# Performance work log

Measured on AMD Instinct MI355X. Metric: run time of the kernel, lower is better.

The kernel has to match this reference:

```python
import jax, jax.numpy as jnp
import numpy as np

B, D, U, M, K = 8192, 512, 512, 16, 64


def setup_inputs() -> dict:
    key = jax.random.key(0)
    ks = jax.random.split(key, 5)
    return {
        "x": jax.random.normal(ks[0], (B, D), dtype=jnp.float32),
        "key_kernel": jax.random.normal(ks[1], (D, K), dtype=jnp.float32) * (1.0 / np.sqrt(D)),
        "key_bias": jnp.zeros((K,), dtype=jnp.float32),
        "keys_map": jax.random.normal(ks[2], (M, K), dtype=jnp.float32),
        "kernels": jax.random.normal(ks[3], (M, D, U), dtype=jnp.float32) * (1.0 / np.sqrt(D)),
        "biases": jnp.zeros((M, U), dtype=jnp.float32),
    }


def reference(x, key_kernel, key_bias, keys_map, kernels, biases):
    # key projection: [B, K]
    keyv = x @ key_kernel + key_bias
    # inverse-distance similarity to mode keys: [B, M]
    dist = jnp.sqrt(jnp.sum((keyv[:, None, :] - keys_map[None, :, :]) ** 2, axis=-1))
    sim = 1.0 / (dist + 1.0)
    modes = kernels.shape[0]
    # kernel = mean_m(sim_m * kernels_m); out = x @ kernel.
    # Distributive identity: out = (1/M) * sum_m sim_m * (x @ kernels_m)
    out = jnp.einsum("bm,bd,mdu->bu", sim, x, kernels) / modes
    # bias = mean_m(sim_m * biases_m): [B, U]
    out = out + (sim @ biases) / modes
    return out
```

## Files before the change

### kernel.cpp

```cpp
#include <hip/hip_runtime.h>
#include <hip/hip_bf16.h>
#include <stdint.h>

#define B_SZ 8192
#define D_SZ 512
#define U_SZ 512
#define M_SZ 16
#define K_SZ 64

typedef short bf16x8 __attribute__((ext_vector_type(8)));
typedef float f32x4 __attribute__((ext_vector_type(4)));

__device__ __forceinline__ unsigned short f2bf(float f) {
  union { float f; unsigned u; } v; v.f = f;
  unsigned r = v.u + 0x7fffu + ((v.u >> 16) & 1u);
  return (unsigned short)(r >> 16);
}

__global__ __launch_bounds__(256) void prep1(
    const float* __restrict__ x, const float* __restrict__ key_kernel,
    const float* __restrict__ kernels, unsigned short* __restrict__ xbf,
    unsigned short* __restrict__ kbf, unsigned short* __restrict__ wkbf) {
  __shared__ float tf[32][65];
  int bid = blockIdx.x;
  int t = threadIdx.x;

  if (bid < 2048) {
    int m = bid >> 7;
    int rem = bid & 127;
    int a = (rem >> 3) & 15;
    int ut = rem & 7;
    int d0 = a * 32, u0 = ut * 64;
    {
      int dr = t >> 4, uc = t & 15;
      const float* src = kernels + ((size_t)m * D_SZ + d0 + dr) * U_SZ + u0 + uc * 4;
      float4 aa = *(const float4*)src;
      float4 bb = *(const float4*)(src + (size_t)16 * U_SZ);
      tf[dr][uc * 4 + 0] = aa.x; tf[dr][uc * 4 + 1] = aa.y;
      tf[dr][uc * 4 + 2] = aa.z; tf[dr][uc * 4 + 3] = aa.w;
      tf[dr + 16][uc * 4 + 0] = bb.x; tf[dr + 16][uc * 4 + 1] = bb.y;
      tf[dr + 16][uc * 4 + 2] = bb.z; tf[dr + 16][uc * 4 + 3] = bb.w;
    }
    __syncthreads();
    {
      int ur = t >> 2, dc = t & 3;
      int j = ur >> 4, lane16 = ur & 15;
      int kt = a >> 1, h = a & 1;
      unsigned short* dst = kbf +
          (((((size_t)m * 8 + ut) * 8 + kt) * 4 + j) * 2 + h) * 512 +
          ((size_t)dc * 16 + lane16) * 8;
      ushort4 lo, hi;
      lo.x = f2bf(tf[dc * 8 + 0][ur]); lo.y = f2bf(tf[dc * 8 + 1][ur]);
      lo.z = f2bf(tf[dc * 8 + 2][ur]); lo.w = f2bf(tf[dc * 8 + 3][ur]);
      hi.x = f2bf(tf[dc * 8 + 4][ur]); hi.y = f2bf(tf[dc * 8 + 5][ur]);
      hi.z = f2bf(tf[dc * 8 + 6][ur]); hi.w = f2bf(tf[dc * 8 + 7][ur]);
      *(ushort4*)dst = lo;
      *(ushort4*)(dst + 4) = hi;
    }
    return;
  }

  if (bid < 2056) {
    int kt = bid - 2048;
#pragma unroll
    for (int rep = 0; rep < 2; ++rep) {
      int c = rep * 256 + t;
      int j = c >> 7, h = (c >> 6) & 1, quad = (c >> 4) & 3, ln = c & 15;
      int dd = kt * 64 + h * 32 + quad * 8;
      int u = j * 16 + ln;
      unsigned short v[8];
#pragma unroll
      for (int e = 0; e < 8; ++e)
        v[e] = f2bf(key_kernel[(size_t)(dd + e) * K_SZ + u]);
      unsigned short* dst =
          wkbf + ((size_t)((kt * 4 + j) * 2 + h) * 64 + quad * 16 + ln) * 8;
#pragma unroll
      for (int e = 0; e < 8; ++e) dst[e] = v[e];
    }
    return;
  }

  int xb0 = bid - 2056;
  int bt = xb0 >> 3, i = xb0 & 7;
  int b0 = xb0 * 16;
#pragma unroll
  for (int rep = 0; rep < 4; ++rep) {
    int idx = rep * 256 + t;
    int kt = idx >> 7, h = (idx >> 6) & 1, quad = (idx >> 4) & 3, ln = idx & 15;
    const float* src = x + (size_t)(b0 + ln) * D_SZ + kt * 64 + h * 32 + quad * 8;
    float4 a = *(const float4*)src;
    float4 b = *(const float4*)(src + 4);
    ushort4 lo, hi;
    lo.x = f2bf(a.x); lo.y = f2bf(a.y); lo.z = f2bf(a.z); lo.w = f2bf(a.w);
    hi.x = f2bf(b.x); hi.y = f2bf(b.y); hi.z = f2bf(b.z); hi.w = f2bf(b.w);
    unsigned short* dst =
        xbf + ((((size_t)bt * 8 + kt) * 8 + i) * 2 + h) * 512 +
        ((size_t)quad * 16 + ln) * 8;
    *(ushort4*)dst = lo;
    *(ushort4*)(dst + 4) = hi;
  }
}

__global__ __launch_bounds__(256) void prep2(
    const unsigned short* __restrict__ xbf, const unsigned short* __restrict__ wkbf,
    const float* __restrict__ key_bias, const float* __restrict__ keys_map,
    float* __restrict__ simT) {
  __shared__ float kv[64][68];
  __shared__ float sKM[16][64];
  int t = threadIdx.x, w = t >> 6, l = t & 63;
  int blk = blockIdx.x;
  int b0 = blk * 64, bt = blk >> 1, ibase = (blk & 1) * 4;
  int lane16 = l & 15, quad = l >> 4;

  ((float4*)sKM)[t] = ((const float4*)keys_map)[t];

  f32x4 acc[4];
#pragma unroll
  for (int j = 0; j < 4; ++j) acc[j] = (f32x4){0.f, 0.f, 0.f, 0.f};

  for (int kt = 0; kt < 8; ++kt) {
    bf16x8 af[2];
#pragma unroll
    for (int h = 0; h < 2; ++h)
      af[h] = *(const bf16x8*)(xbf +
                               ((((size_t)bt * 8 + kt) * 8 + ibase + w) * 2 + h) * 512 +
                               (size_t)l * 8);
#pragma unroll
    for (int j = 0; j < 4; ++j) {
      bf16x8 b0f = *(const bf16x8*)(wkbf + ((size_t)((kt * 4 + j) * 2 + 0) * 64 + l) * 8);
      bf16x8 b1f = *(const bf16x8*)(wkbf + ((size_t)((kt * 4 + j) * 2 + 1) * 64 + l) * 8);
      acc[j] = __builtin_amdgcn_mfma_f32_16x16x32_bf16(af[0], b0f, acc[j], 0, 0, 0);
      acc[j] = __builtin_amdgcn_mfma_f32_16x16x32_bf16(af[1], b1f, acc[j], 0, 0, 0);
    }
  }
#pragma unroll
  for (int j = 0; j < 4; ++j) {
    float bc = key_bias[j * 16 + lane16];
#pragma unroll
    for (int r = 0; r < 4; ++r)
      kv[w * 16 + quad * 4 + r][j * 16 + lane16] = acc[j][r] + bc;
  }
  __syncthreads();

  int row = t >> 2, mg = (t & 3) * 4;
  float d2[4] = {0.f, 0.f, 0.f, 0.f};
#pragma unroll 8
  for (int k = 0; k < 64; ++k) {
    float kvv = kv[row][k];
#pragma unroll
    for (int q = 0; q < 4; ++q) {
      float df = kvv - sKM[mg + q][k];
      d2[q] += df * df;
    }
  }
#pragma unroll
  for (int q = 0; q < 4; ++q)
    simT[(size_t)(mg + q) * B_SZ + b0 + row] = 1.0f / (sqrtf(d2[q]) + 1.0f);
}

__global__ __launch_bounds__(256, 2) void poly_gemm(
    const unsigned short* __restrict__ xbf,
    const unsigned short* __restrict__ kbf,
    const float* __restrict__ simT,
    const float* __restrict__ biases,
    float* __restrict__ out) {
  __shared__ float sRed[8192];

  int t = threadIdx.x, w = t >> 6, l = t & 63;
  int bid = blockIdx.x;
  int ut = bid & 7, bt = bid >> 3;
  int b0 = bt * 128, u0 = ut * 64;
  int half = w >> 1, rw = w & 1;
  int lane16 = l & 15, quad = l >> 4;

  f32x4 facc[4][4];
#pragma unroll
  for (int i = 0; i < 4; ++i)
#pragma unroll
    for (int j = 0; j < 4; ++j) facc[i][j] = (f32x4){0.f, 0.f, 0.f, 0.f};

#pragma unroll 1
  for (int kt = 0; kt < 8; ++kt) {
    bf16x8 af[4][2];
#pragma unroll
    for (int ii = 0; ii < 4; ++ii)
#pragma unroll
      for (int h = 0; h < 2; ++h)
        af[ii][h] = *(const bf16x8*)(
            xbf + ((((size_t)bt * 8 + kt) * 8 + rw * 4 + ii) * 2 + h) * 512 +
            (size_t)l * 8);

#pragma unroll 2
    for (int mi = 0; mi < 8; ++mi) {
      int mode = half * 8 + mi;
      const unsigned short* bb =
          kbf + ((((size_t)mode * 8 + ut) * 8 + kt) * 4) * 2 * 512;
      bf16x8 bfr[4][2];
#pragma unroll
      for (int j = 0; j < 4; ++j)
#pragma unroll
        for (int h = 0; h < 2; ++h)
          bfr[j][h] = *(const bf16x8*)(bb + ((size_t)(j * 2 + h)) * 512 +
                                       (size_t)l * 8);

      f32x4 sv[4];
#pragma unroll
      for (int i = 0; i < 4; ++i)
        sv[i] = *(const f32x4*)(simT + (size_t)mode * B_SZ + b0 + rw * 64 +
                                i * 16 + quad * 4);

#pragma unroll
      for (int i = 0; i < 4; ++i)
#pragma unroll
        for (int j = 0; j < 4; ++j) {
          f32x4 p = __builtin_amdgcn_mfma_f32_16x16x32_bf16(
              af[i][0], bfr[j][0], (f32x4){0.f, 0.f, 0.f, 0.f}, 0, 0, 0);
          p = __builtin_amdgcn_mfma_f32_16x16x32_bf16(af[i][1], bfr[j][1], p,
                                                      0, 0, 0);
#pragma unroll
          for (int r = 0; r < 4; ++r) facc[i][j][r] += sv[i][r] * p[r];
        }

      if (kt == 0) {
        float bbv[4];
#pragma unroll
        for (int j = 0; j < 4; ++j)
          bbv[j] = biases[(size_t)mode * U_SZ + u0 + j * 16 + lane16];
#pragma unroll
        for (int i = 0; i < 4; ++i)
#pragma unroll
          for (int j = 0; j < 4; ++j)
#pragma unroll
            for (int r = 0; r < 4; ++r) facc[i][j][r] += sv[i][r] * bbv[j];
      }
    }
  }

  __syncthreads();
  if (half == 1) {
#pragma unroll
    for (int i = 0; i < 4; ++i)
#pragma unroll
      for (int r = 0; r < 4; ++r)
#pragma unroll
        for (int j = 0; j < 4; ++j)
          sRed[rw * 4096 + (i * 16 + quad * 4 + r) * 64 + j * 16 + lane16] =
              facc[i][j][r];
  }
  __syncthreads();
  if (half == 0) {
#pragma unroll
    for (int i = 0; i < 4; ++i)
#pragma unroll
      for (int r = 0; r < 4; ++r) {
        int row = b0 + rw * 64 + i * 16 + quad * 4 + r;
        float* orow = out + (size_t)row * U_SZ + u0;
#pragma unroll
        for (int j = 0; j < 4; ++j)
          orow[j * 16 + lane16] =
              (facc[i][j][r] +
               sRed[rw * 4096 + (i * 16 + quad * 4 + r) * 64 + j * 16 + lane16]) *
              0.0625f;
      }
  }
}

extern "C" void kernel_launch(void* const* d_in, const int* in_sizes, int n_in,
                              void* d_out, int out_size, void* d_ws, size_t ws_size,
                              hipStream_t stream) {
  const float* x = (const float*)d_in[0];
  const float* key_kernel = (const float*)d_in[1];
  const float* key_bias = (const float*)d_in[2];
  const float* keys_map = (const float*)d_in[3];
  const float* kernels = (const float*)d_in[4];
  const float* biases = (const float*)d_in[5];
  float* out = (float*)d_out;

  char* p = (char*)d_ws;
  unsigned short* xbf = (unsigned short*)p;  p += (size_t)B_SZ * D_SZ * 2;
  unsigned short* kbf = (unsigned short*)p;  p += (size_t)M_SZ * U_SZ * D_SZ * 2;
  unsigned short* wkbf = (unsigned short*)p; p += (size_t)K_SZ * D_SZ * 2;
  float* simT = (float*)p;

  prep1<<<dim3(2568), 256, 0, stream>>>(x, key_kernel, kernels, xbf, kbf, wkbf);
  prep2<<<dim3(128), 256, 0, stream>>>(xbf, wkbf, key_bias, keys_map, simT);
  poly_gemm<<<dim3(512), 256, 0, stream>>>(xbf, kbf, simT, biases, out);
}
```

Measured before the change: 172.2 us.

## Split poly_gemm modes across four wave pairs with 512-thread blocks

Doubles the block size of the main GEMM kernel from 256 to 512 threads so that four wave pairs each handle four of the sixteen modes instead of two pairs handling eight. This raises the number of waves per tile and shortens each wave's serial mode loop. The partial accumulators are then combined through a padded shared-memory buffer in a three-step serialized reduction. The extra barriers and reduction passes add cost, and register pressure under launch_bounds(512,4) may cause spills.

Result: slower. 520.2 us (+202.2%).

```diff
diff --git a/kernel.cpp b/kernel.cpp
--- a/kernel.cpp
+++ b/kernel.cpp
@@ -158,19 +158,19 @@
     simT[(size_t)(mg + q) * B_SZ + b0 + row] = 1.0f / (sqrtf(d2[q]) + 1.0f);
 }
 
-__global__ __launch_bounds__(256, 2) void poly_gemm(
+__global__ __launch_bounds__(512, 4) void poly_gemm(
     const unsigned short* __restrict__ xbf,
     const unsigned short* __restrict__ kbf,
     const float* __restrict__ simT,
     const float* __restrict__ biases,
     float* __restrict__ out) {
-  __shared__ float sRed[8192];
+  __shared__ float sRed[2][64][68];
 
   int t = threadIdx.x, w = t >> 6, l = t & 63;
   int bid = blockIdx.x;
   int ut = bid & 7, bt = bid >> 3;
   int b0 = bt * 128, u0 = ut * 64;
-  int half = w >> 1, rw = w & 1;
+  int q = w >> 1, rw = w & 1;
   int lane16 = l & 15, quad = l >> 4;
 
   f32x4 facc[4][4];
@@ -191,8 +191,8 @@
             (size_t)l * 8);
 
 #pragma unroll 2
-    for (int mi = 0; mi < 8; ++mi) {
-      int mode = half * 8 + mi;
+    for (int mi = 0; mi < 4; ++mi) {
+      int mode = q * 4 + mi;
       const unsigned short* bb =
           kbf + ((((size_t)mode * 8 + ut) * 8 + kt) * 4) * 2 * 512;
       bf16x8 bfr[4][2];
@@ -237,18 +237,37 @@
   }
 
   __syncthreads();
-  if (half == 1) {
+  if (q == 3) {
 #pragma unroll
     for (int i = 0; i < 4; ++i)
 #pragma unroll
       for (int r = 0; r < 4; ++r)
 #pragma unroll
         for (int j = 0; j < 4; ++j)
-          sRed[rw * 4096 + (i * 16 + quad * 4 + r) * 64 + j * 16 + lane16] =
-              facc[i][j][r];
-  }
-  __syncthreads();
-  if (half == 0) {
+          sRed[rw][i * 16 + quad * 4 + r][j * 16 + lane16] = facc[i][j][r];
+  }
+  __syncthreads();
+  if (q == 2) {
+#pragma unroll
+    for (int i = 0; i < 4; ++i)
+#pragma unroll
+      for (int r = 0; r < 4; ++r)
+#pragma unroll
+        for (int j = 0; j < 4; ++j)
+          sRed[rw][i * 16 + quad * 4 + r][j * 16 + lane16] += facc[i][j][r];
+  }
+  __syncthreads();
+  if (q == 1) {
+#pragma unroll
+    for (int i = 0; i < 4; ++i)
+#pragma unroll
+      for (int r = 0; r < 4; ++r)
+#pragma unroll
+        for (int j = 0; j < 4; ++j)
+          sRed[rw][i * 16 + quad * 4 + r][j * 16 + lane16] += facc[i][j][r];
+  }
+  __syncthreads();
+  if (q == 0) {
 #pragma unroll
     for (int i = 0; i < 4; ++i)
 #pragma unroll
@@ -259,7 +278,7 @@
         for (int j = 0; j < 4; ++j)
           orow[j * 16 + lane16] =
               (facc[i][j][r] +
-               sRed[rw * 4096 + (i * 16 + quad * 4 + r) * 64 + j * 16 + lane16]) *
+               sRed[rw][i * 16 + quad * 4 + r][j * 16 + lane16]) *
               0.0625f;
       }
   }
@@ -284,5 +303,5 @@
 
   prep1<<<dim3(2568), 256, 0, stream>>>(x, key_kernel, kernels, xbf, kbf, wkbf);
   prep2<<<dim3(128), 256, 0, stream>>>(xbf, wkbf, key_bias, keys_map, simT);
-  poly_gemm<<<dim3(512), 256, 0, stream>>>(xbf, kbf, simT, biases, out);
-}
+  poly_gemm<<<dim3(512), 512, 0, stream>>>(xbf, kbf, simT, biases, out);
+}
```

## Double-buffer weight tiles into LDS via async global_load_lds

Applied to the files above, without the earlier changes.

The GEMM kernel now streams each per-wave weight slice into a private double-buffered LDS region using global_load_lds, prefetching the next mode/k-tile while computing the current one, with manual vmcnt waits. Similarity and bias values are staged once into shared memory instead of being reloaded from global memory inside the inner loop. The reduction buffer gets padded rows to avoid bank conflicts. LDS use grows to about 76KB and the occupancy hint of 2 is dropped, which may reduce waves per CU. The hand-coded vmcnt counts also depend on the compiler not reordering the other vector-memory loads.

New measurement: 172.7 us. No clear change (+0.3%).

```diff
diff --git a/kernel.cpp b/kernel.cpp
--- a/kernel.cpp
+++ b/kernel.cpp
@@ -158,13 +158,23 @@
     simT[(size_t)(mg + q) * B_SZ + b0 + row] = 1.0f / (sqrtf(d2[q]) + 1.0f);
 }
 
-__global__ __launch_bounds__(256, 2) void poly_gemm(
+__device__ __forceinline__ void stage_slice(const unsigned short* src,
+                                            unsigned short* dst_lds) {
+#pragma unroll
+  for (int c = 0; c < 8; ++c)
+    __builtin_amdgcn_global_load_lds(
+        (const __attribute__((address_space(1))) unsigned int*)(src + c * 512),
+        (__attribute__((address_space(3))) unsigned int*)(dst_lds + c * 512),
+        16, 0, 0);
+}
+
+__global__ __launch_bounds__(256) void poly_gemm(
     const unsigned short* __restrict__ xbf,
     const unsigned short* __restrict__ kbf,
     const float* __restrict__ simT,
     const float* __restrict__ biases,
     float* __restrict__ out) {
-  __shared__ float sRed[8192];
+  __shared__ __align__(16) char smem[77824];
 
   int t = threadIdx.x, w = t >> 6, l = t & 63;
   int bid = blockIdx.x;
@@ -173,11 +183,32 @@
   int half = w >> 1, rw = w & 1;
   int lane16 = l & 15, quad = l >> 4;
 
+  float* sSim = (float*)(smem + 65536);
+  float* sBias = (float*)(smem + 73728);
+  unsigned short* kbuf = (unsigned short*)(smem + w * 16384);
+
+  {
+    int m = t >> 4, c = (t & 15) * 8;
+    const float* src = simT + (size_t)m * B_SZ + b0 + c;
+    float4 a = *(const float4*)src;
+    float4 b = *(const float4*)(src + 4);
+    float4* dst = (float4*)(sSim + m * 128 + c);
+    dst[0] = a; dst[1] = b;
+    int cb = (t & 15) * 4;
+    *(float4*)(sBias + m * 64 + cb) =
+        *(const float4*)(biases + (size_t)m * U_SZ + u0 + cb);
+  }
+  __syncthreads();
+
   f32x4 facc[4][4];
 #pragma unroll
   for (int i = 0; i < 4; ++i)
 #pragma unroll
     for (int j = 0; j < 4; ++j) facc[i][j] = (f32x4){0.f, 0.f, 0.f, 0.f};
+
+  const unsigned short* kbf_l = kbf + (size_t)l * 8;
+
+  stage_slice(kbf_l + ((((size_t)(half * 8) * 8 + ut) * 8) + 0) * 4096, kbuf);
 
 #pragma unroll 1
   for (int kt = 0; kt < 8; ++kt) {
@@ -190,24 +221,33 @@
             xbf + ((((size_t)bt * 8 + kt) * 8 + rw * 4 + ii) * 2 + h) * 512 +
             (size_t)l * 8);
 
-#pragma unroll 2
+#pragma unroll
     for (int mi = 0; mi < 8; ++mi) {
       int mode = half * 8 + mi;
-      const unsigned short* bb =
-          kbf + ((((size_t)mode * 8 + ut) * 8 + kt) * 4) * 2 * 512;
+      {
+        int nmi = (mi + 1) & 7;
+        int nkt = (mi == 7) ? ((kt + 1) & 7) : kt;
+        stage_slice(
+            kbf_l + ((((size_t)(half * 8 + nmi) * 8 + ut) * 8) + nkt) * 4096,
+            kbuf + ((mi + 1) & 1) * 4096);
+      }
+      if (mi == 0)
+        asm volatile("s_waitcnt vmcnt(16)" ::: "memory");
+      else
+        asm volatile("s_waitcnt vmcnt(8)" ::: "memory");
+
+      const unsigned short* lb = kbuf + (mi & 1) * 4096;
       bf16x8 bfr[4][2];
 #pragma unroll
       for (int j = 0; j < 4; ++j)
 #pragma unroll
         for (int h = 0; h < 2; ++h)
-          bfr[j][h] = *(const bf16x8*)(bb + ((size_t)(j * 2 + h)) * 512 +
-                                       (size_t)l * 8);
+          bfr[j][h] = *(const bf16x8*)(lb + (j * 2 + h) * 512 + (size_t)l * 8);
 
       f32x4 sv[4];
 #pragma unroll
       for (int i = 0; i < 4; ++i)
-        sv[i] = *(const f32x4*)(simT + (size_t)mode * B_SZ + b0 + rw * 64 +
-                                i * 16 + quad * 4);
+        sv[i] = *(const f32x4*)(sSim + mode * 128 + rw * 64 + i * 16 + quad * 4);
 
 #pragma unroll
       for (int i = 0; i < 4; ++i)
@@ -225,7 +265,7 @@
         float bbv[4];
 #pragma unroll
         for (int j = 0; j < 4; ++j)
-          bbv[j] = biases[(size_t)mode * U_SZ + u0 + j * 16 + lane16];
+          bbv[j] = sBias[mode * 64 + j * 16 + lane16];
 #pragma unroll
         for (int i = 0; i < 4; ++i)
 #pragma unroll
@@ -236,7 +276,10 @@
     }
   }
 
+  asm volatile("s_waitcnt vmcnt(0)" ::: "memory");
   __syncthreads();
+
+  float* sRed = (float*)smem;
   if (half == 1) {
 #pragma unroll
     for (int i = 0; i < 4; ++i)
@@ -244,7 +287,7 @@
       for (int r = 0; r < 4; ++r)
 #pragma unroll
         for (int j = 0; j < 4; ++j)
-          sRed[rw * 4096 + (i * 16 + quad * 4 + r) * 64 + j * 16 + lane16] =
+          sRed[(rw * 64 + i * 16 + quad * 4 + r) * 68 + j * 16 + lane16] =
               facc[i][j][r];
   }
   __syncthreads();
@@ -259,7 +302,7 @@
         for (int j = 0; j < 4; ++j)
           orow[j * 16 + lane16] =
               (facc[i][j][r] +
-               sRed[rw * 4096 + (i * 16 + quad * 4 + r) * 64 + j * 16 + lane16]) *
+               sRed[(rw * 64 + i * 16 + quad * 4 + r) * 68 + j * 16 + lane16]) *
               0.0625f;
       }
   }
```

## Stage mode kernels in LDS via async global_load_lds with a 4-buffer ring, larger batch tile

Applied to the files above, without the earlier changes.

Each poly_gemm block now covers 256 batch rows, with each wave owning 64 rows across all 16 modes. This removes the cross-half reduction through shared memory and halves the grid. Kernel tiles are streamed into a 4-deep LDS ring with global_load_lds, and the next x fragments are prefetched into registers, so loads overlap the MFMA work. Similarity and bias values are preloaded into LDS. Separately, the x bf16 conversion in prep1 now goes through an LDS transpose for coalesced reads. The costs are occupancy (1 block per CU with about 52 KB of LDS, grid of only 256 blocks) and fragile hand-written vmcnt waits.

Measured after the change: 183.3 us. 6.5% more time.

```diff
diff --git a/kernel.cpp b/kernel.cpp
--- a/kernel.cpp
+++ b/kernel.cpp
@@ -22,6 +22,7 @@
     const float* __restrict__ kernels, unsigned short* __restrict__ xbf,
     unsigned short* __restrict__ kbf, unsigned short* __restrict__ wkbf) {
   __shared__ float tf[32][65];
+  __shared__ unsigned short sx[16][520];
   int bid = blockIdx.x;
   int t = threadIdx.x;
 
@@ -80,24 +81,35 @@
     return;
   }
 
-  int xb0 = bid - 2056;
-  int bt = xb0 >> 3, i = xb0 & 7;
-  int b0 = xb0 * 16;
-#pragma unroll
-  for (int rep = 0; rep < 4; ++rep) {
-    int idx = rep * 256 + t;
-    int kt = idx >> 7, h = (idx >> 6) & 1, quad = (idx >> 4) & 3, ln = idx & 15;
-    const float* src = x + (size_t)(b0 + ln) * D_SZ + kt * 64 + h * 32 + quad * 8;
-    float4 a = *(const float4*)src;
-    float4 b = *(const float4*)(src + 4);
-    ushort4 lo, hi;
-    lo.x = f2bf(a.x); lo.y = f2bf(a.y); lo.z = f2bf(a.z); lo.w = f2bf(a.w);
-    hi.x = f2bf(b.x); hi.y = f2bf(b.y); hi.z = f2bf(b.z); hi.w = f2bf(b.w);
-    unsigned short* dst =
-        xbf + ((((size_t)bt * 8 + kt) * 8 + i) * 2 + h) * 512 +
-        ((size_t)quad * 16 + ln) * 8;
-    *(ushort4*)dst = lo;
-    *(ushort4*)(dst + 4) = hi;
+  {
+    int xb0 = bid - 2056;
+    int btx = xb0 >> 3, i = xb0 & 7;
+    int b0 = xb0 * 16;
+#pragma unroll
+    for (int rep = 0; rep < 8; ++rep) {
+      int idx = rep * 256 + t;
+      int row = idx >> 7;
+      int c4 = (idx & 127) * 4;
+      float4 v = *(const float4*)(x + (size_t)(b0 + row) * D_SZ + c4);
+      ushort4 o;
+      o.x = f2bf(v.x); o.y = f2bf(v.y); o.z = f2bf(v.z); o.w = f2bf(v.w);
+      *(ushort4*)(&sx[row][c4]) = o;
+    }
+    __syncthreads();
+    int w = t >> 6, l = t & 63;
+    int ln = l & 15, quad = l >> 4;
+#pragma unroll
+    for (int rep = 0; rep < 4; ++rep) {
+      int c = w * 4 + rep;
+      int kt = c >> 1, h = c & 1;
+      const unsigned short* srcp = &sx[ln][kt * 64 + h * 32 + quad * 8];
+      ushort4 lo = *(const ushort4*)(srcp);
+      ushort4 hi = *(const ushort4*)(srcp + 4);
+      unsigned short* dst =
+          xbf + ((((size_t)btx * 8 + kt) * 8 + i) * 2 + h) * 512 + (size_t)l * 8;
+      *(ushort4*)dst = lo;
+      *(ushort4*)(dst + 4) = hi;
+    }
   }
 }
 
@@ -158,20 +170,65 @@
     simT[(size_t)(mg + q) * B_SZ + b0 + row] = 1.0f / (sqrtf(d2[q]) + 1.0f);
 }
 
-__global__ __launch_bounds__(256, 2) void poly_gemm(
+#define STAGE(mode_, kt_, bufi_)                                               \
+  {                                                                            \
+    const unsigned short* _src = kbf_l +                                       \
+        (((size_t)(mode_) * 8 + ut) * 8 + (kt_)) * 4096 + w * 1024;            \
+    unsigned short* _dst = Bbuf + (bufi_) * 4096 + w * 1024;                   \
+    __builtin_amdgcn_global_load_lds(                                          \
+        (const __attribute__((address_space(1))) unsigned int*)(_src),         \
+        (__attribute__((address_space(3))) unsigned int*)(_dst), 16, 0, 0);    \
+    __builtin_amdgcn_global_load_lds(                                          \
+        (const __attribute__((address_space(1))) unsigned int*)(_src + 512),   \
+        (__attribute__((address_space(3))) unsigned int*)(_dst + 512), 16, 0,  \
+        0);                                                                    \
+  }
+
+#define LOAD_AF(dst_, kt_)                                                     \
+  _Pragma("unroll") for (int ii = 0; ii < 4; ++ii)                             \
+      _Pragma("unroll") for (int h = 0; h < 2; ++h) dst_[ii][h] =              \
+      *(const bf16x8*)(xbf +                                                   \
+                       ((((size_t)(bt * 2 + (w >> 1)) * 8 + (kt_)) * 8 +       \
+                         (w & 1) * 4 + ii) * 2 + h) * 512 +                    \
+                       (size_t)l * 8);
+
+__global__ __launch_bounds__(256, 1) void poly_gemm(
     const unsigned short* __restrict__ xbf,
     const unsigned short* __restrict__ kbf,
     const float* __restrict__ simT,
     const float* __restrict__ biases,
     float* __restrict__ out) {
-  __shared__ float sRed[8192];
+  __shared__ __align__(16) char smem[53248];
 
   int t = threadIdx.x, w = t >> 6, l = t & 63;
   int bid = blockIdx.x;
   int ut = bid & 7, bt = bid >> 3;
-  int b0 = bt * 128, u0 = ut * 64;
-  int half = w >> 1, rw = w & 1;
+  int b0 = bt * 256, u0 = ut * 64;
   int lane16 = l & 15, quad = l >> 4;
+
+  unsigned short* Bbuf = (unsigned short*)smem;
+  float* sSim = (float*)(smem + 32768);
+  float* sBias = (float*)(smem + 49152);
+
+  {
+    int m = t >> 4, c = t & 15;
+    const float* src = simT + (size_t)m * B_SZ + b0 + c * 16;
+    float4* dst = (float4*)(sSim + m * 256 + c * 16);
+#pragma unroll
+    for (int q = 0; q < 4; ++q) dst[q] = ((const float4*)src)[q];
+    *(float4*)(sBias + m * 64 + c * 4) =
+        *(const float4*)(biases + (size_t)m * U_SZ + u0 + c * 4);
+  }
+
+  const unsigned short* kbf_l = kbf + (size_t)l * 8;
+
+  bf16x8 afc[4][2], afn[4][2];
+
+  STAGE(0, 0, 0);
+  STAGE(1, 0, 1);
+  LOAD_AF(afc, 0);
+  asm volatile("s_waitcnt vmcnt(0)" ::: "memory");
+  __syncthreads();
 
   f32x4 facc[4][4];
 #pragma unroll
@@ -181,88 +238,84 @@
 
 #pragma unroll 1
   for (int kt = 0; kt < 8; ++kt) {
-    bf16x8 af[4][2];
-#pragma unroll
-    for (int ii = 0; ii < 4; ++ii)
-#pragma unroll
-      for (int h = 0; h < 2; ++h)
-        af[ii][h] = *(const bf16x8*)(
-            xbf + ((((size_t)bt * 8 + kt) * 8 + rw * 4 + ii) * 2 + h) * 512 +
-            (size_t)l * 8);
-
-#pragma unroll 2
-    for (int mi = 0; mi < 8; ++mi) {
-      int mode = half * 8 + mi;
-      const unsigned short* bb =
-          kbf + ((((size_t)mode * 8 + ut) * 8 + kt) * 4) * 2 * 512;
-      bf16x8 bfr[4][2];
+#pragma unroll 1
+    for (int mg = 0; mg < 4; ++mg) {
+#pragma unroll
+      for (int mu = 0; mu < 4; ++mu) {
+        const int mode = mg * 4 + mu;
+        {
+          int mode2 = (mode + 2) & 15;
+          int kt2 = (mode >= 14) ? ((kt + 1) & 7) : kt;
+          STAGE(mode2, kt2, (mode + 2) & 3);
+        }
+        if (mode == 0 && kt < 7) { LOAD_AF(afn, kt + 1); }
+        if (mode <= 1 && kt <= 6)
+          asm volatile("s_waitcnt vmcnt(12)" ::: "memory");
+        else
+          asm volatile("s_waitcnt vmcnt(4)" ::: "memory");
+        asm volatile("s_barrier" ::: "memory");
+
+        const unsigned short* lb = Bbuf + (mode & 3) * 4096;
+        bf16x8 bfr[4][2];
+#pragma unroll
+        for (int j = 0; j < 4; ++j)
+#pragma unroll
+          for (int h = 0; h < 2; ++h)
+            bfr[j][h] =
+                *(const bf16x8*)(lb + (j * 2 + h) * 512 + (size_t)l * 8);
+
+        f32x4 sv[4];
+#pragma unroll
+        for (int i = 0; i < 4; ++i)
+          sv[i] = *(const f32x4*)(sSim + mode * 256 + w * 64 + i * 16 +
+                                  quad * 4);
+
+#pragma unroll
+        for (int i = 0; i < 4; ++i)
+#pragma unroll
+          for (int j = 0; j < 4; ++j) {
+            f32x4 p = __builtin_amdgcn_mfma_f32_16x16x32_bf16(
+                afc[i][0], bfr[j][0], (f32x4){0.f, 0.f, 0.f, 0.f}, 0, 0, 0);
+            p = __builtin_amdgcn_mfma_f32_16x16x32_bf16(afc[i][1], bfr[j][1],
+                                                        p, 0, 0, 0);
+#pragma unroll
+            for (int r = 0; r < 4; ++r) facc[i][j][r] += sv[i][r] * p[r];
+          }
+
+        if (kt == 0) {
+          float bbv[4];
+#pragma unroll
+          for (int j = 0; j < 4; ++j)
+            bbv[j] = sBias[mode * 64 + j * 16 + lane16];
+#pragma unroll
+          for (int i = 0; i < 4; ++i)
+#pragma unroll
+            for (int j = 0; j < 4; ++j)
+#pragma unroll
+              for (int r = 0; r < 4; ++r)
+                facc[i][j][r] += sv[i][r] * bbv[j];
+        }
+      }
+    }
+    if (kt < 7) {
+#pragma unroll
+      for (int ii = 0; ii < 4; ++ii)
+#pragma unroll
+        for (int h = 0; h < 2; ++h) afc[ii][h] = afn[ii][h];
+    }
+  }
+
+  asm volatile("s_waitcnt vmcnt(0)" ::: "memory");
+#pragma unroll
+  for (int i = 0; i < 4; ++i)
+#pragma unroll
+    for (int r = 0; r < 4; ++r) {
+      int row = b0 + w * 64 + i * 16 + quad * 4 + r;
+      float* orow = out + (size_t)row * U_SZ + u0;
 #pragma unroll
       for (int j = 0; j < 4; ++j)
-#pragma unroll
-        for (int h = 0; h < 2; ++h)
-          bfr[j][h] = *(const bf16x8*)(bb + ((size_t)(j * 2 + h)) * 512 +
-                                       (size_t)l * 8);
-
-      f32x4 sv[4];
-#pragma unroll
-      for (int i = 0; i < 4; ++i)
-        sv[i] = *(const f32x4*)(simT + (size_t)mode * B_SZ + b0 + rw * 64 +
-                                i * 16 + quad * 4);
-
-#pragma unroll
-      for (int i = 0; i < 4; ++i)
-#pragma unroll
-        for (int j = 0; j < 4; ++j) {
-          f32x4 p = __builtin_amdgcn_mfma_f32_16x16x32_bf16(
-              af[i][0], bfr[j][0], (f32x4){0.f, 0.f, 0.f, 0.f}, 0, 0, 0);
-          p = __builtin_amdgcn_mfma_f32_16x16x32_bf16(af[i][1], bfr[j][1], p,
-                                                      0, 0, 0);
-#pragma unroll
-          for (int r = 0; r < 4; ++r) facc[i][j][r] += sv[i][r] * p[r];
-        }
-
-      if (kt == 0) {
-        float bbv[4];
-#pragma unroll
-        for (int j = 0; j < 4; ++j)
-          bbv[j] = biases[(size_t)mode * U_SZ + u0 + j * 16 + lane16];
-#pragma unroll
-        for (int i = 0; i < 4; ++i)
-#pragma unroll
-          for (int j = 0; j < 4; ++j)
-#pragma unroll
-            for (int r = 0; r < 4; ++r) facc[i][j][r] += sv[i][r] * bbv[j];
-      }
-    }
-  }
-
-  __syncthreads();
-  if (half == 1) {
-#pragma unroll
-    for (int i = 0; i < 4; ++i)
-#pragma unroll
-      for (int r = 0; r < 4; ++r)
-#pragma unroll
-        for (int j = 0; j < 4; ++j)
-          sRed[rw * 4096 + (i * 16 + quad * 4 + r) * 64 + j * 16 + lane16] =
-              facc[i][j][r];
-  }
-  __syncthreads();
-  if (half == 0) {
-#pragma unroll
-    for (int i = 0; i < 4; ++i)
-#pragma unroll
-      for (int r = 0; r < 4; ++r) {
-        int row = b0 + rw * 64 + i * 16 + quad * 4 + r;
-        float* orow = out + (size_t)row * U_SZ + u0;
-#pragma unroll
-        for (int j = 0; j < 4; ++j)
-          orow[j * 16 + lane16] =
-              (facc[i][j][r] +
-               sRed[rw * 4096 + (i * 16 + quad * 4 + r) * 64 + j * 16 + lane16]) *
-              0.0625f;
-      }
-  }
+        orow[j * 16 + lane16] = facc[i][j][r] * 0.0625f;
+    }
 }
 
 extern "C" void kernel_launch(void* const* d_in, const int* in_sizes, int n_in,
@@ -284,5 +337,5 @@
 
   prep1<<<dim3(2568), 256, 0, stream>>>(x, key_kernel, kernels, xbf, kbf, wkbf);
   prep2<<<dim3(128), 256, 0, stream>>>(xbf, wkbf, key_bias, keys_map, simT);
-  poly_gemm<<<dim3(512), 256, 0, stream>>>(xbf, kbf, simT, biases, out);
-}
+  poly_gemm<<<dim3(256), 256, 0, stream>>>(xbf, kbf, simT, biases, out);
+}
```
